# Performance work log

Hardware: AMD Instinct MI355X
Metric: run time of the kernel (lower is better)

## Reference

```python
import jax, jax.numpy as jnp
import numpy as np

LENGTH = 512
Q = 2 * LENGTH + 3   # match + insert + flank/unannotated/terminal states
S = 26               # amino-acid alphabet size


def setup_inputs() -> dict:
    key = jax.random.key(0)
    k1, k2, k3, k4 = jax.random.split(key, 4)
    seq = jax.random.randint(k1, (256, 512), 0, S, dtype=jnp.int32)
    A_logits = jax.random.normal(k2, (Q, Q), dtype=jnp.float32)
    B_logits = jax.random.normal(k3, (Q, S), dtype=jnp.float32)
    init_logits = jax.random.normal(k4, (Q,), dtype=jnp.float32)
    return {"seq": seq, "A_logits": A_logits, "B_logits": B_logits,
            "init_logits": init_logits}


def reference(seq, A_logits, B_logits, init_logits):
    # Row-stochastic transition matrix A [q,q], emission matrix B [q,s],
    # initial state distribution init [q] (cell builds these from kernels
    # via softmax/normalization in make_A()/make_B()).
    A = jax.nn.softmax(A_logits, axis=-1)
    B = jax.nn.softmax(B_logits, axis=-1)
    init = jax.nn.softmax(init_logits)

    # Emission likelihoods per timestep: E[b,t,q] = B[q, seq[b,t]]
    E = B.T[seq]  # [batch, T, q]

    # Scaled HMM forward recursion (log-sum-exp in scaled prob space).
    alpha0 = init[None, :] * E[:, 0]            # [batch, q]
    s0 = jnp.sum(alpha0, axis=-1)               # [batch]
    carry0 = (alpha0 / s0[:, None], jnp.log(s0))

    def step(carry, e_t):
        alpha, ll = carry
        f = (alpha @ A) * e_t                   # [batch, q]
        s = jnp.sum(f, axis=-1)                 # scaling factor
        return (f / s[:, None], ll + jnp.log(s)), None

    E_rest = jnp.transpose(E[:, 1:], (1, 0, 2))  # [T-1, batch, q]
    (alpha, loglik), _ = jax.lax.scan(step, carry0, E_rest)
    return loglik  # per-sequence log-likelihood [batch]
```

## Files before the change

### kernel.cpp

```cpp
#include <hip/hip_runtime.h>
#include <math.h>

typedef __bf16 bf16x8 __attribute__((ext_vector_type(8)));
typedef float f32x4 __attribute__((ext_vector_type(4)));
typedef unsigned int u32x4 __attribute__((ext_vector_type(4)));
typedef unsigned long long u64;

constexpr int QQ = 1027;
constexpr int SS = 26;
constexpr int TT = 512;
constexpr int NB = 256;
constexpr int KP = 1056;
constexpr int NP = 1040;
constexpr int BTS = 1040;
constexpr int NSL = 13;
constexpr int NBB = 16;
constexpr int MB = 16;
constexpr int NWV = 5;
constexpr int CBLK = NWV * 64;
constexpr int KSTEPS = KP / 32;
constexpr int BUFN = NB * NP;
constexpr int BSQ = NP / 4;
constexpr int LQ = 274;
constexpr int TOTQ = MB * BSQ;
constexpr int NLD = TOTQ / CBLK;
constexpr u64 SMASK = 0x7FFF7FFF7FFF7FFFull;

__device__ __forceinline__ unsigned short f2bf(float f) {
  union { float f; unsigned u; } v; v.f = f;
  return (unsigned short)((v.u + 0x7fffu + ((v.u >> 16) & 1u)) >> 16);
}

__device__ __forceinline__ u64 ald8(const u64* p) {
  return __hip_atomic_load((u64*)p, __ATOMIC_RELAXED, __HIP_MEMORY_SCOPE_AGENT);
}
__device__ __forceinline__ void ast8(u64* p, u64 v) {
  __hip_atomic_store(p, v, __ATOMIC_RELAXED, __HIP_MEMORY_SCOPE_AGENT);
}

__device__ __forceinline__ float sum4bf(u64 q) {
  union { unsigned u; float f; } a, b, c, d;
  a.u = ((unsigned)(q & 0xFFFFu)) << 16;
  b.u = ((unsigned)((q >> 16) & 0xFFFFu)) << 16;
  c.u = ((unsigned)((q >> 32) & 0xFFFFu)) << 16;
  d.u = ((unsigned)((q >> 48) & 0xFFFFu)) << 16;
  return (a.f + b.f) + (c.f + d.f);
}

__global__ void k_zero(u32x4* p, int n) {
  int i = blockIdx.x * blockDim.x + threadIdx.x;
  if (i < n) p[i] = (u32x4){0u, 0u, 0u, 0u};
}

__global__ void k_fill(u32x4* p, int n) {
  int i = blockIdx.x * blockDim.x + threadIdx.x;
  if (i < n) p[i] = (u32x4){0x80008000u, 0x80008000u, 0x80008000u, 0x80008000u};
}

__global__ void k_prep_init(const float* __restrict__ il, float* __restrict__ ip) {
  __shared__ float red[1024];
  int tid = threadIdx.x;
  float m = -1e30f;
  for (int q = tid; q < QQ; q += 1024) m = fmaxf(m, il[q]);
  red[tid] = m; __syncthreads();
  for (int off = 512; off > 0; off >>= 1) {
    if (tid < off) red[tid] = fmaxf(red[tid], red[tid + off]);
    __syncthreads();
  }
  m = red[0]; __syncthreads();
  float s = 0.f;
  for (int q = tid; q < QQ; q += 1024) s += expf(il[q] - m);
  red[tid] = s; __syncthreads();
  for (int off = 512; off > 0; off >>= 1) {
    if (tid < off) red[tid] += red[tid + off];
    __syncthreads();
  }
  s = red[0];
  float inv = 1.0f / s;
  for (int q = tid; q < QQ; q += 1024) ip[q] = expf(il[q] - m) * inv;
}

__global__ void k_prep_B(const float* __restrict__ bl, float* __restrict__ bt) {
  int q = blockIdx.x * blockDim.x + threadIdx.x;
  if (q >= QQ) return;
  const float* row = bl + (size_t)q * SS;
  float m = -1e30f;
  for (int c = 0; c < SS; ++c) m = fmaxf(m, row[c]);
  float s = 0.f;
  for (int c = 0; c < SS; ++c) s += expf(row[c] - m);
  float inv = 1.0f / s;
  for (int c = 0; c < SS; ++c) bt[c * BTS + q] = expf(row[c] - m) * inv;
}

__global__ void k_prep_A(const float* __restrict__ al, unsigned short* __restrict__ at) {
  int r = blockIdx.x;
  const float* row = al + (size_t)r * QQ;
  __shared__ float red[256];
  int tid = threadIdx.x;
  float m = -1e30f;
  for (int n = tid; n < QQ; n += 256) m = fmaxf(m, row[n]);
  red[tid] = m; __syncthreads();
  for (int off = 128; off > 0; off >>= 1) {
    if (tid < off) red[tid] = fmaxf(red[tid], red[tid + off]);
    __syncthreads();
  }
  m = red[0]; __syncthreads();
  float s = 0.f;
  for (int n = tid; n < QQ; n += 256) s += expf(row[n] - m);
  red[tid] = s; __syncthreads();
  for (int off = 128; off > 0; off >>= 1) {
    if (tid < off) red[tid] += red[tid + off];
    __syncthreads();
  }
  s = red[0];
  float inv = 1.0f / s;
  for (int n = tid; n < QQ; n += 256) at[(size_t)n * KP + r] = f2bf(expf(row[n] - m) * inv);
}

__global__ void k_init_step(const int* __restrict__ seq, const float* __restrict__ ip,
                            const float* __restrict__ Bt, unsigned short* __restrict__ buf0) {
  int b = blockIdx.x, tid = threadIdx.x;
  int c0 = seq[b * TT];
  for (int q = tid; q < NP; q += 256)
    buf0[(size_t)b * NP + q] = f2bf(ip[q] * Bt[c0 * BTS + q]);
}

__global__ __launch_bounds__(CBLK, 1) void k_hmm_coop(
    const int* __restrict__ seq, const unsigned short* __restrict__ At,
    const float* __restrict__ Bt, unsigned short* __restrict__ bufB,
    float* __restrict__ out) {
  __shared__ u64 aldsq[MB * LQ];
  __shared__ float srowF[MB];

  const int tid = threadIdx.x, wg = blockIdx.x;
  const int bb = wg % NBB, sl = wg / NBB;
  const int lane = tid & 63, wv = tid >> 6;
  const int lrow = lane >> 4, lcol = lane & 15;
  const int n0w = (sl * NWV + wv) * 16;

  if (tid < 64) aldsq[(tid >> 2) * LQ + 260 + (tid & 3)] = 0;

  u32x4 atr[KSTEPS];
  {
    const u32x4* atp = (const u32x4*)(At + (size_t)(n0w + lcol) * KP + 8 * lrow);
#pragma unroll
    for (int ks = 0; ks < KSTEPS; ++ks) atr[ks] = atp[4 * ks];
  }
  const u32x4 ones4 = (u32x4){0x3F803F80u, 0x3F803F80u, 0x3F803F80u, 0x3F803F80u};

  float ll = 0.f;

  for (int t = 1; t < TT; ++t) {
    const int rd = (t - 1) % 3, wri = t % 3;
    const unsigned par = (unsigned)((t - 1) & 1);
    const u64 wtag = (u64)(unsigned)(t & 1) << 15;
    const u64* ain = (const u64*)(bufB + (size_t)rd * BUFN) + (size_t)bb * TOTQ;
    u64* wbuf8 = (u64*)(bufB + (size_t)wri * BUFN);

    const int ch = seq[(bb * MB + lcol) * TT + t];
    const f32x4 ev = *(const f32x4*)(Bt + (size_t)ch * BTS + n0w + 4 * lrow);

    u64 av[NLD];
    const u64* asrc = ain + tid;
#pragma unroll
    for (int j = 0; j < NLD; ++j) av[j] = ald8(asrc + j * CBLK);
    unsigned pend = (1u << NLD) - 1;
    while (true) {
      unsigned np = 0;
#pragma unroll
      for (int j = 0; j < NLD; ++j)
        if ((pend >> j) & 1u)
          if ((unsigned)((av[j] >> 15) & 1ull) != par) np |= 1u << j;
      pend = np;
      if (!pend) break;
      __builtin_amdgcn_s_sleep(1);
#pragma unroll
      for (int j = 0; j < NLD; ++j)
        if ((pend >> j) & 1u) av[j] = ald8(asrc + j * CBLK);
    }
#pragma unroll
    for (int j = 0; j < NLD; ++j) av[j] &= SMASK;

#pragma unroll
    for (int j = 0; j < NLD; ++j) {
      int g = tid + j * CBLK;
      int r = g / BSQ;
      aldsq[r * LQ + (g - r * BSQ)] = av[j];
    }
    __syncthreads();

    const u32x4* ap = ((const u32x4*)aldsq) + lcol * (LQ / 2) + lrow;
    f32x4 acc = (f32x4){0.f, 0.f, 0.f, 0.f};
    f32x4 accs = (f32x4){0.f, 0.f, 0.f, 0.f};
#pragma unroll
    for (int ks = 0; ks < KSTEPS; ++ks) {
      u32x4 af = ap[4 * ks];
      acc = __builtin_amdgcn_mfma_f32_16x16x32_bf16(
          __builtin_bit_cast(bf16x8, atr[ks]), __builtin_bit_cast(bf16x8, af),
          acc, 0, 0, 0);
      accs = __builtin_amdgcn_mfma_f32_16x16x32_bf16(
          __builtin_bit_cast(bf16x8, ones4), __builtin_bit_cast(bf16x8, af),
          accs, 0, 0, 0);
    }

    const float s = accs[0];
    const float inv = 1.0f / s;
    if (sl == 0 && wv == 0) ll += logf(s);

    u64 hv = 0;
#pragma unroll
    for (int i = 0; i < 4; ++i) {
      float v = acc[i] * ev[i] * inv;
      hv |= ((u64)f2bf(v) | wtag) << (16 * i);
    }
    ast8(wbuf8 + (size_t)(bb * MB + lcol) * BSQ + (n0w >> 2) + lrow, hv);
    __syncthreads();
  }

  if (sl == 0) {
    if (tid < MB) srowF[tid] = 0.f;
    __syncthreads();
    const int fs = (TT - 1) % 3;
    const unsigned parF = (unsigned)((TT - 1) & 1);
    const u64* ain = (const u64*)(bufB + (size_t)fs * BUFN) + (size_t)bb * TOTQ;
#pragma unroll
    for (int j = 0; j < NLD; ++j) {
      int g = tid + j * CBLK;
      u64 q = ald8(ain + g);
      while ((unsigned)((q >> 15) & 1ull) != parF) {
        __builtin_amdgcn_s_sleep(1);
        q = ald8(ain + g);
      }
      atomicAdd(&srowF[g / BSQ], sum4bf(q & SMASK));
    }
    __syncthreads();
    if (wv == 0 && lrow == 0) out[bb * MB + lcol] = ll + logf(srowF[lcol]);
  }
}

extern "C" void kernel_launch(void* const* d_in, const int* in_sizes, int n_in,
                              void* d_out, int out_size, void* d_ws, size_t ws_size,
                              hipStream_t stream) {
  const int* seq = (const int*)d_in[0];
  const float* Al = (const float*)d_in[1];
  const float* Bl = (const float*)d_in[2];
  const float* il = (const float*)d_in[3];
  float* out = (float*)d_out;

  char* ws = (char*)d_ws;
  unsigned short* At = (unsigned short*)ws;
  size_t off_bt = (size_t)NP * KP * 2;
  float* Bt = (float*)(ws + off_bt);
  size_t off_ip = off_bt + (size_t)SS * BTS * 4;
  float* ip = (float*)(ws + off_ip);
  size_t off_buf = off_ip + (size_t)NP * 4;
  unsigned short* bufB = (unsigned short*)(ws + off_buf);
  size_t total = off_buf + (size_t)3 * BUFN * 2;
  int n16 = (int)((total + 15) / 16);

  k_zero<<<(n16 + 255) / 256, 256, 0, stream>>>((u32x4*)ws, n16);
  int nf = (int)(((size_t)BUFN * 2) / 16);
  k_fill<<<(nf + 255) / 256, 256, 0, stream>>>(
      (u32x4*)(bufB + (size_t)2 * BUFN), nf);
  k_prep_init<<<1, 1024, 0, stream>>>(il, ip);
  k_prep_B<<<(QQ + 255) / 256, 256, 0, stream>>>(Bl, Bt);
  k_prep_A<<<QQ, 256, 0, stream>>>(Al, At);
  k_init_step<<<NB, 256, 0, stream>>>(seq, ip, Bt, bufB);

  void* args[] = {(void*)&seq, (void*)&At, (void*)&Bt, (void*)&bufB, (void*)&out};
  hipLaunchCooperativeKernel((void*)k_hmm_coop, dim3(NBB * NSL), dim3(CBLK),
                             args, 0, stream);
}
```

Baseline: 1.562 ms.

## Split alpha fetch into two chunks and overlap second wait with first MFMAs

The K dimension of each timestep's alpha vector is split into two column chunks of 120 and 140 quads. The kernel waits only on the first chunk, stages it into LDS and runs the first 15 MFMA k-steps while the second chunk's flags are still being polled. The LDS staging buffer is double-buffered, so the trailing __syncthreads per step is dropped and lighter s_waitcnt+s_barrier calls are used instead. KSTEPS drops from 33 to 33 (1056/32 is the same), so the aim is to overlap inter-workgroup sync latency with compute, at the cost of an extra barrier and more registers.

```diff
diff --git a/kernel.cpp b/kernel.cpp
--- a/kernel.cpp
+++ b/kernel.cpp
@@ -18,12 +18,16 @@
 constexpr int MB = 16;
 constexpr int NWV = 5;
 constexpr int CBLK = NWV * 64;
-constexpr int KSTEPS = KP / 32;
+constexpr int KSTEPS = 33;
+constexpr int KSA = 15;
 constexpr int BUFN = NB * NP;
 constexpr int BSQ = NP / 4;
 constexpr int LQ = 274;
 constexpr int TOTQ = MB * BSQ;
-constexpr int NLD = TOTQ / CBLK;
+constexpr int NLA = 6;
+constexpr int NLB = 7;
+constexpr int CA = 120;
+constexpr int CB = 140;
 constexpr u64 SMASK = 0x7FFF7FFF7FFF7FFFull;
 
 __device__ __forceinline__ unsigned short f2bf(float f) {
@@ -36,6 +40,11 @@
 }
 __device__ __forceinline__ void ast8(u64* p, u64 v) {
   __hip_atomic_store(p, v, __ATOMIC_RELAXED, __HIP_MEMORY_SCOPE_AGENT);
+}
+
+__device__ __forceinline__ void wg_barrier_lds() {
+  asm volatile("s_waitcnt lgkmcnt(0)" ::: "memory");
+  __builtin_amdgcn_s_barrier();
 }
 
 __device__ __forceinline__ float sum4bf(u64 q) {
@@ -129,7 +138,7 @@
     const int* __restrict__ seq, const unsigned short* __restrict__ At,
     const float* __restrict__ Bt, unsigned short* __restrict__ bufB,
     float* __restrict__ out) {
-  __shared__ u64 aldsq[MB * LQ];
+  __shared__ u64 aldsq[2][MB * LQ];
   __shared__ float srowF[MB];
 
   const int tid = threadIdx.x, wg = blockIdx.x;
@@ -138,7 +147,23 @@
   const int lrow = lane >> 4, lcol = lane & 15;
   const int n0w = (sl * NWV + wv) * 16;
 
-  if (tid < 64) aldsq[(tid >> 2) * LQ + 260 + (tid & 3)] = 0;
+  if (tid < 128) aldsq[tid >> 6][((tid >> 2) & 15) * LQ + 260 + (tid & 3)] = 0;
+
+  int offA[NLA], ldsA[NLA], offB[NLB], ldsB[NLB];
+#pragma unroll
+  for (int j = 0; j < NLA; ++j) {
+    int g = tid + j * CBLK;
+    int r = g / CA, c = g - r * CA;
+    offA[j] = r * BSQ + c;
+    ldsA[j] = r * LQ + c;
+  }
+#pragma unroll
+  for (int j = 0; j < NLB; ++j) {
+    int g = tid + j * CBLK;
+    int r = g / CB, c = g - r * CB;
+    offB[j] = r * BSQ + CA + c;
+    ldsB[j] = r * LQ + CA + c;
+  }
 
   u32x4 atr[KSTEPS];
   {
@@ -156,44 +181,53 @@
     const u64 wtag = (u64)(unsigned)(t & 1) << 15;
     const u64* ain = (const u64*)(bufB + (size_t)rd * BUFN) + (size_t)bb * TOTQ;
     u64* wbuf8 = (u64*)(bufB + (size_t)wri * BUFN);
+    u64* buf = aldsq[t & 1];
 
     const int ch = seq[(bb * MB + lcol) * TT + t];
     const f32x4 ev = *(const f32x4*)(Bt + (size_t)ch * BTS + n0w + 4 * lrow);
 
-    u64 av[NLD];
-    const u64* asrc = ain + tid;
-#pragma unroll
-    for (int j = 0; j < NLD; ++j) av[j] = ald8(asrc + j * CBLK);
-    unsigned pend = (1u << NLD) - 1;
+    u64 a[NLA], b[NLB];
+#pragma unroll
+    for (int j = 0; j < NLA; ++j) a[j] = ald8(ain + offA[j]);
+#pragma unroll
+    for (int j = 0; j < NLB; ++j) b[j] = ald8(ain + offB[j]);
+
+    unsigned pend = (1u << NLA) - 1;
     while (true) {
       unsigned np = 0;
 #pragma unroll
-      for (int j = 0; j < NLD; ++j)
+      for (int j = 0; j < NLA; ++j)
         if ((pend >> j) & 1u)
-          if ((unsigned)((av[j] >> 15) & 1ull) != par) np |= 1u << j;
+          if ((unsigned)((a[j] >> 15) & 1ull) != par) np |= 1u << j;
+      if (!np) break;
+      __builtin_amdgcn_s_sleep(1);
+#pragma unroll
+      for (int j = 0; j < NLA; ++j)
+        if ((np >> j) & 1u) a[j] = ald8(ain + offA[j]);
       pend = np;
-      if (!pend) break;
-      __builtin_amdgcn_s_sleep(1);
-#pragma unroll
-      for (int j = 0; j < NLD; ++j)
-        if ((pend >> j) & 1u) av[j] = ald8(asrc + j * CBLK);
-    }
-#pragma unroll
-    for (int j = 0; j < NLD; ++j) av[j] &= SMASK;
-
-#pragma unroll
-    for (int j = 0; j < NLD; ++j) {
-      int g = tid + j * CBLK;
-      int r = g / BSQ;
-      aldsq[r * LQ + (g - r * BSQ)] = av[j];
-    }
-    __syncthreads();
-
-    const u32x4* ap = ((const u32x4*)aldsq) + lcol * (LQ / 2) + lrow;
+    }
+#pragma unroll
+    for (int j = 0; j < NLA; ++j) a[j] &= SMASK;
+
+    {
+      unsigned pb = 0;
+#pragma unroll
+      for (int j = 0; j < NLB; ++j)
+        if ((unsigned)((b[j] >> 15) & 1ull) != par) pb |= 1u << j;
+#pragma unroll
+      for (int j = 0; j < NLB; ++j)
+        if ((pb >> j) & 1u) b[j] = ald8(ain + offB[j]);
+    }
+
+#pragma unroll
+    for (int j = 0; j < NLA; ++j) buf[ldsA[j]] = a[j];
+    wg_barrier_lds();
+
+    const u32x4* ap = ((const u32x4*)buf) + lcol * (LQ / 2) + lrow;
     f32x4 acc = (f32x4){0.f, 0.f, 0.f, 0.f};
     f32x4 accs = (f32x4){0.f, 0.f, 0.f, 0.f};
 #pragma unroll
-    for (int ks = 0; ks < KSTEPS; ++ks) {
+    for (int ks = 0; ks < KSA; ++ks) {
       u32x4 af = ap[4 * ks];
       acc = __builtin_amdgcn_mfma_f32_16x16x32_bf16(
           __builtin_bit_cast(bf16x8, atr[ks]), __builtin_bit_cast(bf16x8, af),
@@ -203,6 +237,38 @@
           accs, 0, 0, 0);
     }
 
+    pend = (1u << NLB) - 1;
+    while (true) {
+      unsigned np = 0;
+#pragma unroll
+      for (int j = 0; j < NLB; ++j)
+        if ((pend >> j) & 1u)
+          if ((unsigned)((b[j] >> 15) & 1ull) != par) np |= 1u << j;
+      if (!np) break;
+      __builtin_amdgcn_s_sleep(1);
+#pragma unroll
+      for (int j = 0; j < NLB; ++j)
+        if ((np >> j) & 1u) b[j] = ald8(ain + offB[j]);
+      pend = np;
+    }
+#pragma unroll
+    for (int j = 0; j < NLB; ++j) b[j] &= SMASK;
+
+#pragma unroll
+    for (int j = 0; j < NLB; ++j) buf[ldsB[j]] = b[j];
+    wg_barrier_lds();
+
+#pragma unroll
+    for (int ks = KSA; ks < KSTEPS; ++ks) {
+      u32x4 af = ap[4 * ks];
+      acc = __builtin_amdgcn_mfma_f32_16x16x32_bf16(
+          __builtin_bit_cast(bf16x8, atr[ks]), __builtin_bit_cast(bf16x8, af),
+          acc, 0, 0, 0);
+      accs = __builtin_amdgcn_mfma_f32_16x16x32_bf16(
+          __builtin_bit_cast(bf16x8, ones4), __builtin_bit_cast(bf16x8, af),
+          accs, 0, 0, 0);
+    }
+
     const float s = accs[0];
     const float inv = 1.0f / s;
     if (sl == 0 && wv == 0) ll += logf(s);
@@ -214,7 +280,6 @@
       hv |= ((u64)f2bf(v) | wtag) << (16 * i);
     }
     ast8(wbuf8 + (size_t)(bb * MB + lcol) * BSQ + (n0w >> 2) + lrow, hv);
-    __syncthreads();
   }
 
   if (sl == 0) {
@@ -223,15 +288,17 @@
     const int fs = (TT - 1) % 3;
     const unsigned parF = (unsigned)((TT - 1) & 1);
     const u64* ain = (const u64*)(bufB + (size_t)fs * BUFN) + (size_t)bb * TOTQ;
-#pragma unroll
-    for (int j = 0; j < NLD; ++j) {
+    for (int j = 0; j < NLA + NLB; ++j) {
       int g = tid + j * CBLK;
-      u64 q = ald8(ain + g);
+      if (g >= TOTQ) break;
+      int r = g / BSQ, c = g - r * BSQ;
+      const u64* p = ain + r * BSQ + c;
+      u64 q = ald8(p);
       while ((unsigned)((q >> 15) & 1ull) != parF) {
         __builtin_amdgcn_s_sleep(1);
-        q = ald8(ain + g);
+        q = ald8(p);
       }
-      atomicAdd(&srowF[g / BSQ], sum4bf(q & SMASK));
+      atomicAdd(&srowF[r], sum4bf(q & SMASK));
     }
     __syncthreads();
     if (wv == 0 && lrow == 0) out[bb * MB + lcol] = ll + logf(srowF[lcol]);
```

New measurement: 2.317 ms. 1.48x slower.

## Interleave alpha buffer by state-quad, double-buffer LDS, drop trailing barrier

Applied to the files above, without the earlier changes.

Reorders the global alpha exchange buffer so that the 16 batch rows of each state quad sit next to each other. This lets each thread fetch 16-byte vectors with plain volatile loads, falling back to atomic loads only after several polling rounds. LDS staging is double-buffered by step parity, so the second __syncthreads per step is removed. KSTEPS drops from 33 to a literal 33 (same value). The changes aim to cut polling latency, memory-transaction count and barrier overhead in the per-timestep cross-block synchronisation. The risk is that volatile non-atomic 16-byte loads may observe torn tag bits, and the ordering with one barrier relies on the triple-buffered global scheme.

```diff
diff --git a/kernel.cpp b/kernel.cpp
--- a/kernel.cpp
+++ b/kernel.cpp
@@ -18,12 +18,14 @@
 constexpr int MB = 16;
 constexpr int NWV = 5;
 constexpr int CBLK = NWV * 64;
-constexpr int KSTEPS = KP / 32;
-constexpr int BUFN = NB * NP;
+constexpr int KSTEPS = 33;
 constexpr int BSQ = NP / 4;
+constexpr int TOTQ = MB * BSQ;
+constexpr int BUFQ = NBB * TOTQ;
 constexpr int LQ = 274;
-constexpr int TOTQ = MB * BSQ;
-constexpr int NLD = TOTQ / CBLK;
+constexpr int NPAIR = TOTQ / 2;
+constexpr int PFULL = 6;
+constexpr int PREM = NPAIR - PFULL * CBLK;
 constexpr u64 SMASK = 0x7FFF7FFF7FFF7FFFull;
 
 __device__ __forceinline__ unsigned short f2bf(float f) {
@@ -120,16 +122,18 @@
 __global__ void k_init_step(const int* __restrict__ seq, const float* __restrict__ ip,
                             const float* __restrict__ Bt, unsigned short* __restrict__ buf0) {
   int b = blockIdx.x, tid = threadIdx.x;
+  int bb = b >> 4, brow = b & 15;
   int c0 = seq[b * TT];
+  unsigned short* dst = buf0 + (size_t)bb * TOTQ * 4;
   for (int q = tid; q < NP; q += 256)
-    buf0[(size_t)b * NP + q] = f2bf(ip[q] * Bt[c0 * BTS + q]);
+    dst[(size_t)((q >> 2) * MB + brow) * 4 + (q & 3)] = f2bf(ip[q] * Bt[c0 * BTS + q]);
 }
 
 __global__ __launch_bounds__(CBLK, 1) void k_hmm_coop(
     const int* __restrict__ seq, const unsigned short* __restrict__ At,
     const float* __restrict__ Bt, unsigned short* __restrict__ bufB,
     float* __restrict__ out) {
-  __shared__ u64 aldsq[MB * LQ];
+  __shared__ u64 aldsq[2][MB * LQ];
   __shared__ float srowF[MB];
 
   const int tid = threadIdx.x, wg = blockIdx.x;
@@ -138,7 +142,7 @@
   const int lrow = lane >> 4, lcol = lane & 15;
   const int n0w = (sl * NWV + wv) * 16;
 
-  if (tid < 64) aldsq[(tid >> 2) * LQ + 260 + (tid & 3)] = 0;
+  if (tid < 128) aldsq[tid >> 6][((tid >> 2) & 15) * LQ + 260 + (tid & 3)] = 0;
 
   u32x4 atr[KSTEPS];
   {
@@ -148,48 +152,75 @@
   }
   const u32x4 ones4 = (u32x4){0x3F803F80u, 0x3F803F80u, 0x3F803F80u, 0x3F803F80u};
 
+  const bool has7 = (tid < PREM);
   float ll = 0.f;
 
   for (int t = 1; t < TT; ++t) {
     const int rd = (t - 1) % 3, wri = t % 3;
     const unsigned par = (unsigned)((t - 1) & 1);
     const u64 wtag = (u64)(unsigned)(t & 1) << 15;
-    const u64* ain = (const u64*)(bufB + (size_t)rd * BUFN) + (size_t)bb * TOTQ;
-    u64* wbuf8 = (u64*)(bufB + (size_t)wri * BUFN);
-
+    const u64* ain = (const u64*)bufB + (size_t)rd * BUFQ + (size_t)bb * TOTQ;
+    u64* wbuf8 = (u64*)bufB + (size_t)wri * BUFQ + (size_t)bb * TOTQ;
+    u64* buf = aldsq[t & 1];
+
+    u64 av[14];
+    {
+      const u32x4* vp = (const u32x4*)ain;
+#pragma unroll
+      for (int j = 0; j < PFULL; ++j) {
+        u32x4 v = *(volatile const u32x4*)(vp + tid + j * CBLK);
+        av[2 * j] = (u64)v[0] | ((u64)v[1] << 32);
+        av[2 * j + 1] = (u64)v[2] | ((u64)v[3] << 32);
+      }
+      if (has7) {
+        u32x4 v = *(volatile const u32x4*)(vp + PFULL * CBLK + tid);
+        av[12] = (u64)v[0] | ((u64)v[1] << 32);
+        av[13] = (u64)v[2] | ((u64)v[3] << 32);
+      }
+    }
     const int ch = seq[(bb * MB + lcol) * TT + t];
     const f32x4 ev = *(const f32x4*)(Bt + (size_t)ch * BTS + n0w + 4 * lrow);
 
-    u64 av[NLD];
-    const u64* asrc = ain + tid;
-#pragma unroll
-    for (int j = 0; j < NLD; ++j) av[j] = ald8(asrc + j * CBLK);
-    unsigned pend = (1u << NLD) - 1;
-    while (true) {
-      unsigned np = 0;
-#pragma unroll
-      for (int j = 0; j < NLD; ++j)
-        if ((pend >> j) & 1u)
-          if ((unsigned)((av[j] >> 15) & 1ull) != par) np |= 1u << j;
-      pend = np;
-      if (!pend) break;
-      __builtin_amdgcn_s_sleep(1);
-#pragma unroll
-      for (int j = 0; j < NLD; ++j)
-        if ((pend >> j) & 1u) av[j] = ald8(asrc + j * CBLK);
-    }
-#pragma unroll
-    for (int j = 0; j < NLD; ++j) av[j] &= SMASK;
-
-#pragma unroll
-    for (int j = 0; j < NLD; ++j) {
-      int g = tid + j * CBLK;
-      int r = g / BSQ;
-      aldsq[r * LQ + (g - r * BSQ)] = av[j];
-    }
-    __syncthreads();
-
-    const u32x4* ap = ((const u32x4*)aldsq) + lcol * (LQ / 2) + lrow;
+    {
+      unsigned pend = has7 ? 0x3FFFu : 0x0FFFu;
+      int round = 0;
+      while (true) {
+        unsigned np = 0;
+#pragma unroll
+        for (int w = 0; w < 14; ++w)
+          if ((pend >> w) & 1u)
+            if ((unsigned)((av[w] >> 15) & 1ull) != par) np |= 1u << w;
+        if (!np) break;
+        __builtin_amdgcn_s_sleep(1);
+        ++round;
+        const bool esc = (round >= 8);
+#pragma unroll
+        for (int w = 0; w < 14; ++w)
+          if ((np >> w) & 1u) {
+            int idx = (w < 12) ? (2 * (tid + (w >> 1) * CBLK) + (w & 1))
+                               : (2 * (PFULL * CBLK + tid) + (w & 1));
+            av[w] = esc ? ald8(ain + idx) : *(volatile const u64*)(ain + idx);
+          }
+        pend = np;
+      }
+    }
+
+#pragma unroll
+    for (int j = 0; j < PFULL; ++j) {
+      int p = tid + j * CBLK;
+      int brow = (2 * p) & 15, cq = p >> 3;
+      buf[brow * LQ + cq] = av[2 * j] & SMASK;
+      buf[(brow + 1) * LQ + cq] = av[2 * j + 1] & SMASK;
+    }
+    if (has7) {
+      int p = PFULL * CBLK + tid;
+      int brow = (2 * p) & 15, cq = p >> 3;
+      buf[brow * LQ + cq] = av[12] & SMASK;
+      buf[(brow + 1) * LQ + cq] = av[13] & SMASK;
+    }
+    __syncthreads();
+
+    const u32x4* ap = ((const u32x4*)buf) + lcol * (LQ / 2) + lrow;
     f32x4 acc = (f32x4){0.f, 0.f, 0.f, 0.f};
     f32x4 accs = (f32x4){0.f, 0.f, 0.f, 0.f};
 #pragma unroll
@@ -213,8 +244,7 @@
       float v = acc[i] * ev[i] * inv;
       hv |= ((u64)f2bf(v) | wtag) << (16 * i);
     }
-    ast8(wbuf8 + (size_t)(bb * MB + lcol) * BSQ + (n0w >> 2) + lrow, hv);
-    __syncthreads();
+    ast8(wbuf8 + (size_t)(((n0w >> 2) + lrow) * MB + lcol), hv);
   }
 
   if (sl == 0) {
@@ -222,16 +252,16 @@
     __syncthreads();
     const int fs = (TT - 1) % 3;
     const unsigned parF = (unsigned)((TT - 1) & 1);
-    const u64* ain = (const u64*)(bufB + (size_t)fs * BUFN) + (size_t)bb * TOTQ;
-#pragma unroll
-    for (int j = 0; j < NLD; ++j) {
+    const u64* ain = (const u64*)bufB + (size_t)fs * BUFQ + (size_t)bb * TOTQ;
+#pragma unroll
+    for (int j = 0; j < 13; ++j) {
       int g = tid + j * CBLK;
       u64 q = ald8(ain + g);
       while ((unsigned)((q >> 15) & 1ull) != parF) {
         __builtin_amdgcn_s_sleep(1);
         q = ald8(ain + g);
       }
-      atomicAdd(&srowF[g / BSQ], sum4bf(q & SMASK));
+      atomicAdd(&srowF[g & 15], sum4bf(q & SMASK));
     }
     __syncthreads();
     if (wv == 0 && lrow == 0) out[bb * MB + lcol] = ll + logf(srowF[lcol]);
@@ -255,13 +285,13 @@
   float* ip = (float*)(ws + off_ip);
   size_t off_buf = off_ip + (size_t)NP * 4;
   unsigned short* bufB = (unsigned short*)(ws + off_buf);
-  size_t total = off_buf + (size_t)3 * BUFN * 2;
+  size_t total = off_buf + (size_t)3 * BUFQ * 8;
   int n16 = (int)((total + 15) / 16);
 
   k_zero<<<(n16 + 255) / 256, 256, 0, stream>>>((u32x4*)ws, n16);
-  int nf = (int)(((size_t)BUFN * 2) / 16);
+  int nf = (int)(((size_t)BUFQ * 8) / 16);
   k_fill<<<(nf + 255) / 256, 256, 0, stream>>>(
-      (u32x4*)(bufB + (size_t)2 * BUFN), nf);
+      (u32x4*)((u64*)bufB + (size_t)2 * BUFQ), nf);
   k_prep_init<<<1, 1024, 0, stream>>>(il, ip);
   k_prep_B<<<(QQ + 255) / 256, 256, 0, stream>>>(Bl, Bt);
   k_prep_A<<<QQ, 256, 0, stream>>>(Al, At);
```

Measured after the change: 2.561 ms. +63.9%, slower.

## Interleave alpha buffer by batch row, double-buffer LDS, drop trailing barrier

Applied to the files above, without the earlier changes.

Changes the global alpha exchange buffer layout so each 8-byte quad is interleaved across the 16 batch rows, which makes the per-step reads and writes more contiguous and turns the LDS scatter index into shifts instead of a division. The shared staging array becomes double-buffered by step parity, so the second __syncthreads per timestep can be removed. KSTEPS is hardcoded to 33, which equals KP/32, and the polling loop is reordered slightly. This trades a small amount of extra LDS for one fewer block barrier per step, but the write pattern now scatters each wave's stores across rows.

```diff
diff --git a/kernel.cpp b/kernel.cpp
--- a/kernel.cpp
+++ b/kernel.cpp
@@ -18,11 +18,11 @@
 constexpr int MB = 16;
 constexpr int NWV = 5;
 constexpr int CBLK = NWV * 64;
-constexpr int KSTEPS = KP / 32;
-constexpr int BUFN = NB * NP;
+constexpr int KSTEPS = 33;
 constexpr int BSQ = NP / 4;
+constexpr int TOTQ = MB * BSQ;
+constexpr int BUFQ = NBB * TOTQ;
 constexpr int LQ = 274;
-constexpr int TOTQ = MB * BSQ;
 constexpr int NLD = TOTQ / CBLK;
 constexpr u64 SMASK = 0x7FFF7FFF7FFF7FFFull;
 
@@ -120,16 +120,18 @@
 __global__ void k_init_step(const int* __restrict__ seq, const float* __restrict__ ip,
                             const float* __restrict__ Bt, unsigned short* __restrict__ buf0) {
   int b = blockIdx.x, tid = threadIdx.x;
+  int bb = b >> 4, brow = b & 15;
   int c0 = seq[b * TT];
+  unsigned short* dst = buf0 + (size_t)bb * TOTQ * 4;
   for (int q = tid; q < NP; q += 256)
-    buf0[(size_t)b * NP + q] = f2bf(ip[q] * Bt[c0 * BTS + q]);
+    dst[(size_t)((q >> 2) * MB + brow) * 4 + (q & 3)] = f2bf(ip[q] * Bt[c0 * BTS + q]);
 }
 
 __global__ __launch_bounds__(CBLK, 1) void k_hmm_coop(
     const int* __restrict__ seq, const unsigned short* __restrict__ At,
     const float* __restrict__ Bt, unsigned short* __restrict__ bufB,
     float* __restrict__ out) {
-  __shared__ u64 aldsq[MB * LQ];
+  __shared__ u64 aldsq[2][MB * LQ];
   __shared__ float srowF[MB];
 
   const int tid = threadIdx.x, wg = blockIdx.x;
@@ -138,7 +140,7 @@
   const int lrow = lane >> 4, lcol = lane & 15;
   const int n0w = (sl * NWV + wv) * 16;
 
-  if (tid < 64) aldsq[(tid >> 2) * LQ + 260 + (tid & 3)] = 0;
+  if (tid < 128) aldsq[tid >> 6][((tid >> 2) & 15) * LQ + 260 + (tid & 3)] = 0;
 
   u32x4 atr[KSTEPS];
   {
@@ -154,8 +156,9 @@
     const int rd = (t - 1) % 3, wri = t % 3;
     const unsigned par = (unsigned)((t - 1) & 1);
     const u64 wtag = (u64)(unsigned)(t & 1) << 15;
-    const u64* ain = (const u64*)(bufB + (size_t)rd * BUFN) + (size_t)bb * TOTQ;
-    u64* wbuf8 = (u64*)(bufB + (size_t)wri * BUFN);
+    const u64* ain = (const u64*)bufB + (size_t)rd * BUFQ + (size_t)bb * TOTQ;
+    u64* wbuf8 = (u64*)bufB + (size_t)wri * BUFQ + (size_t)bb * TOTQ;
+    u64* buf = aldsq[t & 1];
 
     const int ch = seq[(bb * MB + lcol) * TT + t];
     const f32x4 ev = *(const f32x4*)(Bt + (size_t)ch * BTS + n0w + 4 * lrow);
@@ -171,12 +174,12 @@
       for (int j = 0; j < NLD; ++j)
         if ((pend >> j) & 1u)
           if ((unsigned)((av[j] >> 15) & 1ull) != par) np |= 1u << j;
+      if (!np) break;
+      __builtin_amdgcn_s_sleep(1);
+#pragma unroll
+      for (int j = 0; j < NLD; ++j)
+        if ((np >> j) & 1u) av[j] = ald8(asrc + j * CBLK);
       pend = np;
-      if (!pend) break;
-      __builtin_amdgcn_s_sleep(1);
-#pragma unroll
-      for (int j = 0; j < NLD; ++j)
-        if ((pend >> j) & 1u) av[j] = ald8(asrc + j * CBLK);
     }
 #pragma unroll
     for (int j = 0; j < NLD; ++j) av[j] &= SMASK;
@@ -184,12 +187,11 @@
 #pragma unroll
     for (int j = 0; j < NLD; ++j) {
       int g = tid + j * CBLK;
-      int r = g / BSQ;
-      aldsq[r * LQ + (g - r * BSQ)] = av[j];
-    }
-    __syncthreads();
-
-    const u32x4* ap = ((const u32x4*)aldsq) + lcol * (LQ / 2) + lrow;
+      buf[(g & 15) * LQ + (g >> 4)] = av[j];
+    }
+    __syncthreads();
+
+    const u32x4* ap = ((const u32x4*)buf) + lcol * (LQ / 2) + lrow;
     f32x4 acc = (f32x4){0.f, 0.f, 0.f, 0.f};
     f32x4 accs = (f32x4){0.f, 0.f, 0.f, 0.f};
 #pragma unroll
@@ -213,8 +215,7 @@
       float v = acc[i] * ev[i] * inv;
       hv |= ((u64)f2bf(v) | wtag) << (16 * i);
     }
-    ast8(wbuf8 + (size_t)(bb * MB + lcol) * BSQ + (n0w >> 2) + lrow, hv);
-    __syncthreads();
+    ast8(wbuf8 + (size_t)(((n0w >> 2) + lrow) * MB + lcol), hv);
   }
 
   if (sl == 0) {
@@ -222,7 +223,7 @@
     __syncthreads();
     const int fs = (TT - 1) % 3;
     const unsigned parF = (unsigned)((TT - 1) & 1);
-    const u64* ain = (const u64*)(bufB + (size_t)fs * BUFN) + (size_t)bb * TOTQ;
+    const u64* ain = (const u64*)bufB + (size_t)fs * BUFQ + (size_t)bb * TOTQ;
 #pragma unroll
     for (int j = 0; j < NLD; ++j) {
       int g = tid + j * CBLK;
@@ -231,7 +232,7 @@
         __builtin_amdgcn_s_sleep(1);
         q = ald8(ain + g);
       }
-      atomicAdd(&srowF[g / BSQ], sum4bf(q & SMASK));
+      atomicAdd(&srowF[g & 15], sum4bf(q & SMASK));
     }
     __syncthreads();
     if (wv == 0 && lrow == 0) out[bb * MB + lcol] = ll + logf(srowF[lcol]);
@@ -255,13 +256,13 @@
   float* ip = (float*)(ws + off_ip);
   size_t off_buf = off_ip + (size_t)NP * 4;
   unsigned short* bufB = (unsigned short*)(ws + off_buf);
-  size_t total = off_buf + (size_t)3 * BUFN * 2;
+  size_t total = off_buf + (size_t)3 * BUFQ * 8;
   int n16 = (int)((total + 15) / 16);
 
   k_zero<<<(n16 + 255) / 256, 256, 0, stream>>>((u32x4*)ws, n16);
-  int nf = (int)(((size_t)BUFN * 2) / 16);
+  int nf = (int)(((size_t)BUFQ * 8) / 16);
   k_fill<<<(nf + 255) / 256, 256, 0, stream>>>(
-      (u32x4*)(bufB + (size_t)2 * BUFN), nf);
+      (u32x4*)((u64*)bufB + (size_t)2 * BUFQ), nf);
   k_prep_init<<<1, 1024, 0, stream>>>(il, ip);
   k_prep_B<<<(QQ + 255) / 256, 256, 0, stream>>>(Bl, Bt);
   k_prep_A<<<QQ, 256, 0, stream>>>(Al, At);
```

Result: slower. 1.837 ms (+17.6%).
